# Kernel tuning notes

Hardware: AMD Instinct MI355X
Metric: run time of the kernel (lower is better)

Reference implementation:

```python
import jax, jax.numpy as jnp
import numpy as np

MARGIN = 1.0


def setup_inputs() -> dict:
    key = jax.random.key(0)
    k1, k2, k3 = jax.random.split(key, 3)
    N, F = 4096, 512
    a = jax.random.normal(k1, (N, F), dtype=jnp.float32)
    b = jax.random.normal(k2, (N, F), dtype=jnp.float32)
    labels = jax.random.randint(k3, (N,), 0, 16, dtype=jnp.int32)
    return {"a": a, "b": b, "labels": labels}


def reference(a, b, labels):
    # D[i, j] = ||b_i - a_j||  (torch: Xa=a[None], Xb=b[:,None], sum over feat)
    # GEMM form of the pairwise sqdist; clamp tiny fp negatives before sqrt.
    Dsq = (jnp.sum(b * b, axis=1)[:, None]
           + jnp.sum(a * a, axis=1)[None, :]
           - 2.0 * (b @ a.T))
    D = jnp.sqrt(jnp.maximum(Dsq, 0.0))            # [N, N]
    Dexpm = jnp.exp(MARGIN - D)                    # [N, N]

    same = labels[:, None] == labels[None, :]      # [N, N]
    eye = jnp.eye(labels.shape[0], dtype=bool)
    pos_mask = same & ~eye                         # ordered positive pairs (i, j)
    neg_mask = ~same                               # negative pairs (labels differ)

    # neg_i sum for row i: sum_k Dexpm[i, k] over k with labels[k] != labels[i]
    row_negsum = jnp.sum(jnp.where(neg_mask, Dexpm, 0.0), axis=1)  # [N]

    # J_ij = log(neg_ik_sum + neg_jl_sum) + D[i, j]; hinged and squared
    J = jnp.log(row_negsum[:, None] + row_negsum[None, :]) + D
    hinge_sq = jnp.square(jnp.maximum(J, 0.0))

    num_pos = jnp.sum(pos_mask)
    return jnp.sum(jnp.where(pos_mask, hinge_sq, 0.0)) / (2.0 * num_pos)
```

## Files before the change

kernel.cpp:

```cpp
#include <hip/hip_runtime.h>
#include <math.h>

#define NROW 4096
#define FDIM 512
#define MARGIN 1.0f
#define NLAB 16
#define PREP_BLK 1024

typedef __attribute__((ext_vector_type(8))) short short8;
typedef __attribute__((ext_vector_type(4))) float floatx4;

__device__ inline unsigned short f2bf(float x) {
    unsigned u = __float_as_uint(x);
    return (unsigned short)((u + 0x7FFFu + ((u >> 16) & 1u)) >> 16);
}
__device__ inline void glds16(const unsigned short* g, unsigned short* l) {
    __builtin_amdgcn_global_load_lds(
        (const __attribute__((address_space(1))) unsigned int*)g,
        (__attribute__((address_space(3))) unsigned int*)l, 16, 0, 0);
}
#define WAIT_VM_BARRIER(N)                                          \
    do {                                                            \
        asm volatile("s_waitcnt vmcnt(" #N ")" ::: "memory");       \
        __builtin_amdgcn_s_barrier();                               \
        __builtin_amdgcn_sched_barrier(0);                          \
    } while (0)

__device__ inline float fast_sqrt_pos(float dsq) {
    float c = fmaxf(dsq, 1e-20f);
    return c * __frsqrt_rn(c);
}

__global__ __launch_bounds__(256) void prep_kernel(
    const float* __restrict__ a, const float* __restrict__ b,
    const int* __restrict__ labels,
    unsigned short* __restrict__ abf, unsigned short* __restrict__ bbf,
    float* __restrict__ na, float* __restrict__ nb,
    float* __restrict__ rns, float* __restrict__ loss,
    int* __restrict__ perm, int* __restrict__ goff,
    int* __restrict__ wl, int* __restrict__ wlmeta) {
    const int t = threadIdx.x;

    if (blockIdx.x == PREP_BLK) {
        __shared__ int hist[NLAB], off[NLAB], cur[NLAB];
        if (t < NLAB) hist[t] = 0;
        __syncthreads();
        for (int i = t; i < NROW; i += 256) atomicAdd(&hist[labels[i] & 15], 1);
        __syncthreads();
        if (t == 0) {
            int acc = 0;
            for (int g = 0; g < NLAB; ++g) { off[g] = acc; acc += hist[g]; }
            int n = 0;
            long long np = 0;
            for (int g = 0; g < NLAB; ++g) {
                goff[g] = off[g];
                int c = hist[g];
                np += (long long)c * (long long)(c - 1);
                int nt = (c + 63) >> 6;
                for (int ti = 0; ti < nt; ++ti)
                    for (int tj = 0; tj < nt; ++tj)
                        wl[n++] = (g << 12) | (ti << 6) | tj;
            }
            goff[NLAB] = NROW;
            wlmeta[0] = n;
            wlmeta[1] = (int)np;
            wlmeta[2] = 0;
            loss[0]   = 0.f;
        }
        __syncthreads();
        if (t < NLAB) cur[t] = off[t];
        __syncthreads();
        for (int i = t; i < NROW; i += 256) {
            int pos = atomicAdd(&cur[labels[i] & 15], 1);
            perm[pos] = i;
        }
        return;
    }

    const int grp = t >> 6;
    const int ln  = t & 63;
    const int row = blockIdx.x * 4 + grp;
    const float4* a4 = (const float4*)(a + (size_t)row * FDIM);
    const float4* b4 = (const float4*)(b + (size_t)row * FDIM);
    const int f = ln * 2;
    float4 va0 = a4[f], va1 = a4[f + 1];
    float4 vb0 = b4[f], vb1 = b4[f + 1];
    float sa = va0.x * va0.x + va0.y * va0.y + va0.z * va0.z + va0.w * va0.w
             + va1.x * va1.x + va1.y * va1.y + va1.z * va1.z + va1.w * va1.w;
    float sb = vb0.x * vb0.x + vb0.y * vb0.y + vb0.z * vb0.z + vb0.w * vb0.w
             + vb1.x * vb1.x + vb1.y * vb1.y + vb1.z * vb1.z + vb1.w * vb1.w;
    short8 ua, ub;
    ua[0] = (short)f2bf(va0.x); ua[1] = (short)f2bf(va0.y);
    ua[2] = (short)f2bf(va0.z); ua[3] = (short)f2bf(va0.w);
    ua[4] = (short)f2bf(va1.x); ua[5] = (short)f2bf(va1.y);
    ua[6] = (short)f2bf(va1.z); ua[7] = (short)f2bf(va1.w);
    ub[0] = (short)f2bf(vb0.x); ub[1] = (short)f2bf(vb0.y);
    ub[2] = (short)f2bf(vb0.z); ub[3] = (short)f2bf(vb0.w);
    ub[4] = (short)f2bf(vb1.x); ub[5] = (short)f2bf(vb1.y);
    ub[6] = (short)f2bf(vb1.z); ub[7] = (short)f2bf(vb1.w);
    *(short8*)&abf[(size_t)row * FDIM + (size_t)f * 4] = ua;
    *(short8*)&bbf[(size_t)row * FDIM + (size_t)f * 4] = ub;
    #pragma unroll
    for (int o = 32; o > 0; o >>= 1) {
        sa += __shfl_down(sa, o);
        sb += __shfl_down(sb, o);
    }
    if (ln == 0) {
        na[row] = sa;
        nb[row] = sb;
        rns[row] = 0.f;
    }
}

__global__ __launch_bounds__(512, 2) void pass_neg(
    const unsigned short* __restrict__ abf, const unsigned short* __restrict__ bbf,
    const int* __restrict__ labels,
    const float* __restrict__ na, const float* __restrict__ nb,
    float* __restrict__ rns)
{
    __shared__ __align__(16) unsigned short arena[65536];
    __shared__ float rpart[4][256];

    const int t    = threadIdx.x;
    const int lane = t & 63;
    const int w    = t >> 6;
    const int wi   = w >> 2;
    const int wj   = w & 3;
    const int lr   = lane & 15;
    const int lq   = lane >> 4;

    const int bid = blockIdx.x;
    const int xcd = bid & 7, loc = bid >> 3;
    const int by  = (xcd >> 1) * 4 + (loc >> 3);
    const int bx  = (xcd & 1) * 8 + (loc & 7);
    const int ti  = by * 256;
    const int tj  = bx * 256;

    floatx4 acc[8][4];
    #pragma unroll
    for (int i = 0; i < 8; ++i)
        #pragma unroll
        for (int j = 0; j < 4; ++j)
            acc[i][j] = (floatx4){0.f, 0.f, 0.f, 0.f};

    auto stage = [&](int s) {
        unsigned short* As = arena + (s & 3) * 16384;
        unsigned short* Bs = As + 8192;
        const int kk = s * 32;
        #pragma unroll
        for (int l = 0; l < 2; ++l) {
            int c   = t + l * 512;
            int row = c >> 2;
            int qs  = (c & 3) ^ ((row >> 1) & 3);
            glds16(abf + (size_t)(tj + row) * FDIM + kk + qs * 8, As + c * 8);
            glds16(bbf + (size_t)(ti + row) * FDIM + kk + qs * 8, Bs + c * 8);
        }
    };

    stage(0);
    stage(1);
    WAIT_VM_BARRIER(0);

    #pragma unroll
    for (int p = 0; p < 8; ++p) {
        if (p < 7) { stage(2 * p + 2); stage(2 * p + 3); }

        #pragma unroll
        for (int ss = 0; ss < 2; ++ss) {
            const int s = 2 * p + ss;
            const unsigned short* As = arena + (s & 3) * 16384;
            const unsigned short* Bs = As + 8192;
            short8 af[8], bv[4];
            #pragma unroll
            for (int ri = 0; ri < 8; ++ri) {
                int R = wi * 128 + ri * 16 + lr;
                af[ri] = *(const short8*)
                    &Bs[R * 32 + ((lq ^ ((R >> 1) & 3))) * 8];
            }
            #pragma unroll
            for (int rj = 0; rj < 4; ++rj) {
                int R = wj * 64 + rj * 16 + lr;
                bv[rj] = *(const short8*)
                    &As[R * 32 + ((lq ^ ((R >> 1) & 3))) * 8];
            }
            __builtin_amdgcn_s_setprio(1);
            #pragma unroll
            for (int ri = 0; ri < 8; ++ri)
                #pragma unroll
                for (int rj = 0; rj < 4; ++rj)
                    acc[ri][rj] = __builtin_amdgcn_mfma_f32_16x16x32_bf16(
                        af[ri], bv[rj], acc[ri][rj], 0, 0, 0);
            __builtin_amdgcn_s_setprio(0);
        }

        if (p < 7) WAIT_VM_BARRIER(0);
    }

    int   ljv[4]; float najv[4];
    #pragma unroll
    for (int rj = 0; rj < 4; ++rj) {
        int jl = wj * 64 + rj * 16 + lr;
        ljv[rj]  = labels[tj + jl];
        najv[rj] = na[tj + jl];
    }
    #pragma unroll
    for (int ri = 0; ri < 8; ++ri) {
        float rs[4] = {0.f, 0.f, 0.f, 0.f};
        int liv[4]; float nbv[4];
        #pragma unroll
        for (int r = 0; r < 4; ++r) {
            int il = wi * 128 + ri * 16 + lq * 4 + r;
            liv[r] = labels[ti + il];
            nbv[r] = nb[ti + il];
        }
        #pragma unroll
        for (int rj = 0; rj < 4; ++rj)
            #pragma unroll
            for (int r = 0; r < 4; ++r) {
                float dsq  = nbv[r] + najv[rj] - 2.f * acc[ri][rj][r];
                float D    = fast_sqrt_pos(dsq);
                float mask = (liv[r] != ljv[rj]) ? 1.f : 0.f;
                rs[r] = fmaf(mask, __expf(MARGIN - D), rs[r]);
            }
        #pragma unroll
        for (int r = 0; r < 4; ++r) {
            #pragma unroll
            for (int o = 8; o > 0; o >>= 1) rs[r] += __shfl_down(rs[r], o, 16);
        }
        if (lr == 0) {
            #pragma unroll
            for (int r = 0; r < 4; ++r)
                rpart[wj][wi * 128 + ri * 16 + lq * 4 + r] = rs[r];
        }
    }
    __syncthreads();
    if (t < 256) {
        float s = rpart[0][t] + rpart[1][t] + rpart[2][t] + rpart[3][t];
        atomicAdd(&rns[ti + t], s);
    }
}

__global__ __launch_bounds__(256) void pass2_pos(
    const unsigned short* __restrict__ abf, const unsigned short* __restrict__ bbf,
    const float* __restrict__ na, const float* __restrict__ nb,
    const float* __restrict__ rns,
    const int* __restrict__ perm, const int* __restrict__ goff,
    const int* __restrict__ wl, const int* __restrict__ wlmeta,
    float* __restrict__ loss_sum, int* __restrict__ done,
    float* __restrict__ out)
{
    __shared__ __align__(16) unsigned short arena[65536];
    __shared__ int   rows_i[64], rows_j[64];
    __shared__ float rbi_s[64], rbj_s[64], nbi_s[64], naj_s[64];
    __shared__ float part[4];

    const int t    = threadIdx.x;
    const int lane = t & 63;
    const int w    = t >> 6;
    const int wi   = w >> 1, wj = w & 1;
    const int lr   = lane & 15;
    const int lq   = lane >> 4;
    const int nwl  = wlmeta[0];

    float local = 0.f;

    for (int item = blockIdx.x; item < nwl; item += gridDim.x) {
        __syncthreads();
        int e  = wl[item];
        int g  = e >> 12, ti = (e >> 6) & 63, tj = e & 63;
        int gb = goff[g], ge = goff[g + 1];
        int cnt = ge - gb;

        if (t < 64) {
            int idx = gb + ti * 64 + t;
            int ig  = perm[idx < ge ? idx : gb];
            rows_i[t] = ig;
            rbi_s[t]  = rns[ig];
            nbi_s[t]  = nb[ig];
        } else if (t < 128) {
            int u   = t - 64;
            int idx = gb + tj * 64 + u;
            int jg  = perm[idx < ge ? idx : gb];
            rows_j[u] = jg;
            rbj_s[u]  = rns[jg];
            naj_s[u]  = na[jg];
        }
        __syncthreads();

        #pragma unroll
        for (int l = 0; l < 16; ++l) {
            int c   = t + l * 256;
            int row = c >> 6;
            int qs  = (c & 63) ^ (row & 7);
            glds16(abf + (size_t)rows_j[row] * FDIM + qs * 8, arena + c * 8);
            glds16(bbf + (size_t)rows_i[row] * FDIM + qs * 8,
                   arena + 32768 + c * 8);
        }
        WAIT_VM_BARRIER(0);

        floatx4 acc[2][2];
        #pragma unroll
        for (int i = 0; i < 2; ++i)
            #pragma unroll
            for (int j = 0; j < 2; ++j)
                acc[i][j] = (floatx4){0.f, 0.f, 0.f, 0.f};

        const unsigned short* As = arena;
        const unsigned short* Bs = arena + 32768;
        #pragma unroll
        for (int ks = 0; ks < 16; ++ks) {
            short8 af[2], bfv[2];
            #pragma unroll
            for (int ri = 0; ri < 2; ++ri) {
                int R  = wi * 32 + ri * 16 + lr;
                int cs = (ks * 4 + lq) ^ (R & 7);
                af[ri] = *(const short8*)&Bs[R * 512 + cs * 8];
            }
            #pragma unroll
            for (int rj = 0; rj < 2; ++rj) {
                int R  = wj * 32 + rj * 16 + lr;
                int cs = (ks * 4 + lq) ^ (R & 7);
                bfv[rj] = *(const short8*)&As[R * 512 + cs * 8];
            }
            #pragma unroll
            for (int ri = 0; ri < 2; ++ri)
                #pragma unroll
                for (int rj = 0; rj < 2; ++rj)
                    acc[ri][rj] = __builtin_amdgcn_mfma_f32_16x16x32_bf16(
                        af[ri], bfv[rj], acc[ri][rj], 0, 0, 0);
        }

        #pragma unroll
        for (int ri = 0; ri < 2; ++ri)
            #pragma unroll
            for (int rj = 0; rj < 2; ++rj) {
                int  jl  = wj * 32 + rj * 16 + lr;
                bool vj  = (tj * 64 + jl) < cnt;
                int  jg  = rows_j[jl];
                float nav = naj_s[jl], rbj = rbj_s[jl];
                #pragma unroll
                for (int r = 0; r < 4; ++r) {
                    int  il = wi * 32 + ri * 16 + lq * 4 + r;
                    bool vi = (ti * 64 + il) < cnt;
                    if (vi && vj && rows_i[il] != jg) {
                        float dsq = nbi_s[il] + nav - 2.f * acc[ri][rj][r];
                        float D   = fast_sqrt_pos(dsq);
                        float J   = __logf(rbi_s[il] + rbj) + D;
                        float h   = fmaxf(J, 0.f);
                        local += h * h;
                    }
                }
            }
    }

    #pragma unroll
    for (int o = 32; o > 0; o >>= 1) local += __shfl_down(local, o);
    if (lane == 0) part[w] = local;
    __syncthreads();
    if (t == 0) {
        atomicAdd(loss_sum, part[0] + part[1] + part[2] + part[3]);
        __threadfence();
        int old = atomicAdd(done, 1);
        if (old == (int)gridDim.x - 1) {
            __threadfence();
            float total = *(volatile float*)loss_sum;
            out[0] = total / (2.0f * (float)wlmeta[1]);
        }
    }
}

extern "C" void kernel_launch(void* const* d_in, const int* in_sizes, int n_in,
                              void* d_out, int out_size, void* d_ws, size_t ws_size,
                              hipStream_t stream) {
    const float* a      = (const float*)d_in[0];
    const float* b      = (const float*)d_in[1];
    const int*   labels = (const int*)d_in[2];
    float* out = (float*)d_out;

    unsigned short* abf = (unsigned short*)d_ws;
    unsigned short* bbf = abf + (size_t)NROW * FDIM;
    float* fws  = (float*)(bbf + (size_t)NROW * FDIM);
    float* na   = fws;
    float* nb   = fws + NROW;
    float* rns  = fws + 2 * NROW;
    float* loss = fws + 3 * NROW;
    int* iws    = (int*)(fws + 3 * NROW + 4);
    int* perm   = iws;
    int* goff   = iws + NROW;
    int* wlmeta = iws + NROW + 20;
    int* wl     = iws + NROW + 24;

    prep_kernel<<<PREP_BLK + 1, 256, 0, stream>>>(a, b, labels, abf, bbf,
                                                  na, nb, rns, loss,
                                                  perm, goff, wl, wlmeta);
    pass_neg<<<(NROW / 256) * (NROW / 256), 512, 0, stream>>>(abf, bbf, labels,
                                                              na, nb, rns);
    pass2_pos<<<256, 256, 0, stream>>>(abf, bbf, na, nb, rns, perm, goff, wl,
                                       wlmeta, loss, &wlmeta[2], out);
}
```

Before: 130.1 us.

## Double waves per block in both GEMM passes and deepen the neg-pass pipeline

pass_neg now runs 1024 threads (16 waves) per 256x256 tile, so each wave owns a 64x64 sub-tile instead of 128x64. The k-loop now prefetches three stages ahead with one load per thread and partial vmcnt waits. The block-to-tile mapping across XCDs is also simplified. pass2_pos moves to 512 threads with a 32x16 sub-tile per wave. The aim is more latency hiding and more waves in flight, at the cost of fewer MFMAs per LDS fragment load, more barrier participants, and a new register budget from the changed launch bounds.

```diff
diff --git a/kernel.cpp b/kernel.cpp
--- a/kernel.cpp
+++ b/kernel.cpp
@@ -112,7 +112,7 @@
     }
 }
 
-__global__ __launch_bounds__(512, 2) void pass_neg(
+__global__ __launch_bounds__(1024, 4) void pass_neg(
     const unsigned short* __restrict__ abf, const unsigned short* __restrict__ bbf,
     const int* __restrict__ labels,
     const float* __restrict__ na, const float* __restrict__ nb,
@@ -130,70 +130,71 @@
     const int lq   = lane >> 4;
 
     const int bid = blockIdx.x;
-    const int xcd = bid & 7, loc = bid >> 3;
-    const int by  = (xcd >> 1) * 4 + (loc >> 3);
-    const int bx  = (xcd & 1) * 8 + (loc & 7);
+    const int wg  = (bid & 7) * 32 + (bid >> 3);
+    const int by  = wg >> 4, bx = wg & 15;
     const int ti  = by * 256;
     const int tj  = bx * 256;
 
-    floatx4 acc[8][4];
-    #pragma unroll
-    for (int i = 0; i < 8; ++i)
+    floatx4 acc[4][4];
+    #pragma unroll
+    for (int i = 0; i < 4; ++i)
         #pragma unroll
         for (int j = 0; j < 4; ++j)
             acc[i][j] = (floatx4){0.f, 0.f, 0.f, 0.f};
+
+    const int srow = t >> 2;
+    const int sqs  = (t & 3) ^ ((srow >> 1) & 3);
+    const unsigned offA = (unsigned)(tj + srow) * FDIM + sqs * 8;
+    const unsigned offB = (unsigned)(ti + srow) * FDIM + sqs * 8;
 
     auto stage = [&](int s) {
         unsigned short* As = arena + (s & 3) * 16384;
         unsigned short* Bs = As + 8192;
         const int kk = s * 32;
-        #pragma unroll
-        for (int l = 0; l < 2; ++l) {
-            int c   = t + l * 512;
-            int row = c >> 2;
-            int qs  = (c & 3) ^ ((row >> 1) & 3);
-            glds16(abf + (size_t)(tj + row) * FDIM + kk + qs * 8, As + c * 8);
-            glds16(bbf + (size_t)(ti + row) * FDIM + kk + qs * 8, Bs + c * 8);
-        }
+        glds16(abf + offA + kk, As + t * 8);
+        glds16(bbf + offB + kk, Bs + t * 8);
     };
 
     stage(0);
     stage(1);
-    WAIT_VM_BARRIER(0);
-
-    #pragma unroll
-    for (int p = 0; p < 8; ++p) {
-        if (p < 7) { stage(2 * p + 2); stage(2 * p + 3); }
-
-        #pragma unroll
-        for (int ss = 0; ss < 2; ++ss) {
-            const int s = 2 * p + ss;
-            const unsigned short* As = arena + (s & 3) * 16384;
-            const unsigned short* Bs = As + 8192;
-            short8 af[8], bv[4];
-            #pragma unroll
-            for (int ri = 0; ri < 8; ++ri) {
-                int R = wi * 128 + ri * 16 + lr;
-                af[ri] = *(const short8*)
-                    &Bs[R * 32 + ((lq ^ ((R >> 1) & 3))) * 8];
-            }
-            #pragma unroll
-            for (int rj = 0; rj < 4; ++rj) {
-                int R = wj * 64 + rj * 16 + lr;
-                bv[rj] = *(const short8*)
-                    &As[R * 32 + ((lq ^ ((R >> 1) & 3))) * 8];
-            }
-            __builtin_amdgcn_s_setprio(1);
-            #pragma unroll
-            for (int ri = 0; ri < 8; ++ri)
-                #pragma unroll
-                for (int rj = 0; rj < 4; ++rj)
-                    acc[ri][rj] = __builtin_amdgcn_mfma_f32_16x16x32_bf16(
-                        af[ri], bv[rj], acc[ri][rj], 0, 0, 0);
-            __builtin_amdgcn_s_setprio(0);
-        }
-
-        if (p < 7) WAIT_VM_BARRIER(0);
+    stage(2);
+    WAIT_VM_BARRIER(4);
+
+    #pragma unroll
+    for (int it = 0; it < 16; ++it) {
+        if (it < 13) stage(it + 3);
+
+        const unsigned short* As = arena + (it & 3) * 16384;
+        const unsigned short* Bs = As + 8192;
+        short8 af[4], bv[4];
+        #pragma unroll
+        for (int ri = 0; ri < 4; ++ri) {
+            int R = wi * 64 + ri * 16 + lr;
+            af[ri] = *(const short8*)
+                &Bs[R * 32 + ((lq ^ ((R >> 1) & 3))) * 8];
+        }
+        #pragma unroll
+        for (int rj = 0; rj < 4; ++rj) {
+            int R = wj * 64 + rj * 16 + lr;
+            bv[rj] = *(const short8*)
+                &As[R * 32 + ((lq ^ ((R >> 1) & 3))) * 8];
+        }
+        __builtin_amdgcn_s_setprio(1);
+        #pragma unroll
+        for (int ri = 0; ri < 4; ++ri)
+            #pragma unroll
+            for (int rj = 0; rj < 4; ++rj)
+                acc[ri][rj] = __builtin_amdgcn_mfma_f32_16x16x32_bf16(
+                    af[ri], bv[rj], acc[ri][rj], 0, 0, 0);
+        __builtin_amdgcn_s_setprio(0);
+
+        if (it < 13) {
+            WAIT_VM_BARRIER(4);
+        } else if (it == 13) {
+            WAIT_VM_BARRIER(2);
+        } else if (it == 14) {
+            WAIT_VM_BARRIER(0);
+        }
     }
 
     int   ljv[4]; float najv[4];
@@ -204,12 +205,12 @@
         najv[rj] = na[tj + jl];
     }
     #pragma unroll
-    for (int ri = 0; ri < 8; ++ri) {
+    for (int ri = 0; ri < 4; ++ri) {
         float rs[4] = {0.f, 0.f, 0.f, 0.f};
         int liv[4]; float nbv[4];
         #pragma unroll
         for (int r = 0; r < 4; ++r) {
-            int il = wi * 128 + ri * 16 + lq * 4 + r;
+            int il = wi * 64 + ri * 16 + lq * 4 + r;
             liv[r] = labels[ti + il];
             nbv[r] = nb[ti + il];
         }
@@ -230,7 +231,7 @@
         if (lr == 0) {
             #pragma unroll
             for (int r = 0; r < 4; ++r)
-                rpart[wj][wi * 128 + ri * 16 + lq * 4 + r] = rs[r];
+                rpart[wj][wi * 64 + ri * 16 + lq * 4 + r] = rs[r];
         }
     }
     __syncthreads();
@@ -240,7 +241,7 @@
     }
 }
 
-__global__ __launch_bounds__(256) void pass2_pos(
+__global__ __launch_bounds__(512) void pass2_pos(
     const unsigned short* __restrict__ abf, const unsigned short* __restrict__ bbf,
     const float* __restrict__ na, const float* __restrict__ nb,
     const float* __restrict__ rns,
@@ -252,12 +253,13 @@
     __shared__ __align__(16) unsigned short arena[65536];
     __shared__ int   rows_i[64], rows_j[64];
     __shared__ float rbi_s[64], rbj_s[64], nbi_s[64], naj_s[64];
-    __shared__ float part[4];
+    __shared__ float part[8];
 
     const int t    = threadIdx.x;
     const int lane = t & 63;
     const int w    = t >> 6;
-    const int wi   = w >> 1, wj = w & 1;
+    const int wi   = w >> 2;
+    const int wj   = w & 3;
     const int lr   = lane & 15;
     const int lq   = lane >> 4;
     const int nwl  = wlmeta[0];
@@ -288,8 +290,8 @@
         __syncthreads();
 
         #pragma unroll
-        for (int l = 0; l < 16; ++l) {
-            int c   = t + l * 256;
+        for (int l = 0; l < 8; ++l) {
+            int c   = t + l * 512;
             int row = c >> 6;
             int qs  = (c & 63) ^ (row & 7);
             glds16(abf + (size_t)rows_j[row] * FDIM + qs * 8, arena + c * 8);
@@ -298,59 +300,51 @@
         }
         WAIT_VM_BARRIER(0);
 
-        floatx4 acc[2][2];
-        #pragma unroll
-        for (int i = 0; i < 2; ++i)
-            #pragma unroll
-            for (int j = 0; j < 2; ++j)
-                acc[i][j] = (floatx4){0.f, 0.f, 0.f, 0.f};
+        floatx4 acc[2];
+        acc[0] = (floatx4){0.f, 0.f, 0.f, 0.f};
+        acc[1] = (floatx4){0.f, 0.f, 0.f, 0.f};
 
         const unsigned short* As = arena;
         const unsigned short* Bs = arena + 32768;
         #pragma unroll
         for (int ks = 0; ks < 16; ++ks) {
-            short8 af[2], bfv[2];
+            short8 af[2], bv;
             #pragma unroll
             for (int ri = 0; ri < 2; ++ri) {
                 int R  = wi * 32 + ri * 16 + lr;
                 int cs = (ks * 4 + lq) ^ (R & 7);
                 af[ri] = *(const short8*)&Bs[R * 512 + cs * 8];
             }
-            #pragma unroll
-            for (int rj = 0; rj < 2; ++rj) {
-                int R  = wj * 32 + rj * 16 + lr;
+            {
+                int R  = wj * 16 + lr;
                 int cs = (ks * 4 + lq) ^ (R & 7);
-                bfv[rj] = *(const short8*)&As[R * 512 + cs * 8];
+                bv = *(const short8*)&As[R * 512 + cs * 8];
             }
             #pragma unroll
             for (int ri = 0; ri < 2; ++ri)
-                #pragma unroll
-                for (int rj = 0; rj < 2; ++rj)
-                    acc[ri][rj] = __builtin_amdgcn_mfma_f32_16x16x32_bf16(
-                        af[ri], bfv[rj], acc[ri][rj], 0, 0, 0);
-        }
-
-        #pragma unroll
-        for (int ri = 0; ri < 2; ++ri)
-            #pragma unroll
-            for (int rj = 0; rj < 2; ++rj) {
-                int  jl  = wj * 32 + rj * 16 + lr;
-                bool vj  = (tj * 64 + jl) < cnt;
-                int  jg  = rows_j[jl];
-                float nav = naj_s[jl], rbj = rbj_s[jl];
-                #pragma unroll
-                for (int r = 0; r < 4; ++r) {
-                    int  il = wi * 32 + ri * 16 + lq * 4 + r;
-                    bool vi = (ti * 64 + il) < cnt;
-                    if (vi && vj && rows_i[il] != jg) {
-                        float dsq = nbi_s[il] + nav - 2.f * acc[ri][rj][r];
-                        float D   = fast_sqrt_pos(dsq);
-                        float J   = __logf(rbi_s[il] + rbj) + D;
-                        float h   = fmaxf(J, 0.f);
-                        local += h * h;
-                    }
+                acc[ri] = __builtin_amdgcn_mfma_f32_16x16x32_bf16(
+                    af[ri], bv, acc[ri], 0, 0, 0);
+        }
+
+        int  jl  = wj * 16 + lr;
+        bool vj  = (tj * 64 + jl) < cnt;
+        int  jg  = rows_j[jl];
+        float nav = naj_s[jl], rbj = rbj_s[jl];
+        #pragma unroll
+        for (int ri = 0; ri < 2; ++ri) {
+            #pragma unroll
+            for (int r = 0; r < 4; ++r) {
+                int  il = wi * 32 + ri * 16 + lq * 4 + r;
+                bool vi = (ti * 64 + il) < cnt;
+                if (vi && vj && rows_i[il] != jg) {
+                    float dsq = nbi_s[il] + nav - 2.f * acc[ri][r];
+                    float D   = fast_sqrt_pos(dsq);
+                    float J   = __logf(rbi_s[il] + rbj) + D;
+                    float h   = fmaxf(J, 0.f);
+                    local += h * h;
                 }
             }
+        }
     }
 
     #pragma unroll
@@ -358,7 +352,10 @@
     if (lane == 0) part[w] = local;
     __syncthreads();
     if (t == 0) {
-        atomicAdd(loss_sum, part[0] + part[1] + part[2] + part[3]);
+        float s = 0.f;
+        #pragma unroll
+        for (int i = 0; i < 8; ++i) s += part[i];
+        atomicAdd(loss_sum, s);
         __threadfence();
         int old = atomicAdd(done, 1);
         if (old == (int)gridDim.x - 1) {
@@ -393,8 +390,8 @@
     prep_kernel<<<PREP_BLK + 1, 256, 0, stream>>>(a, b, labels, abf, bbf,
                                                   na, nb, rns, loss,
                                                   perm, goff, wl, wlmeta);
-    pass_neg<<<(NROW / 256) * (NROW / 256), 512, 0, stream>>>(abf, bbf, labels,
-                                                              na, nb, rns);
-    pass2_pos<<<256, 256, 0, stream>>>(abf, bbf, na, nb, rns, perm, goff, wl,
+    pass_neg<<<(NROW / 256) * (NROW / 256), 1024, 0, stream>>>(abf, bbf, labels,
+                                                               na, nb, rns);
+    pass2_pos<<<256, 512, 0, stream>>>(abf, bbf, na, nb, rns, perm, goff, wl,
                                        wlmeta, loss, &wlmeta[2], out);
 }
```

Measured after the change: 123.0 us. 5.4% less time.
